# Kernel optimization log

Hardware: AMD Instinct MI355X
Metric: run time of the kernel (lower is better)

## Reference

```python
import jax, jax.numpy as jnp
import numpy as np

N = 100000        # nodes
E = 1600000       # edges (avg degree 16)
F_IN = 128        # num_node_features
H = 64            # hidden_channels
F_EDGE = 8        # num_edge_features (output dim per edge)


def setup_inputs() -> dict:
    key = jax.random.key(0)
    ks = jax.random.split(key, 9)
    x = jax.random.normal(ks[0], (N, F_IN), dtype=jnp.float32)
    edge_index = jax.random.randint(ks[1], (2, E), 0, N, dtype=jnp.int32)
    s = 0.05
    W1 = jax.random.normal(ks[2], (F_IN, H), jnp.float32) * s
    b1 = jnp.zeros((H,), jnp.float32)
    W2 = jax.random.normal(ks[3], (H, H), jnp.float32) * s
    b2 = jnp.zeros((H,), jnp.float32)
    Wl = jax.random.normal(ks[4], (2 * H, F_EDGE), jnp.float32) * s
    bl = jnp.zeros((F_EDGE,), jnp.float32)
    return {"x": x, "edge_index": edge_index,
            "W1": W1, "b1": b1, "W2": W2, "b2": b2, "Wl": Wl, "bl": bl}


def gcn_conv(x, W, b, row, col, n):
    # GCNConv: h = D^{-1/2} (A + I) D^{-1/2} (x W) + b
    h = x @ W
    sl = jnp.arange(n, dtype=row.dtype)          # self-loops
    r = jnp.concatenate([row, sl])
    c = jnp.concatenate([col, sl])
    ones = jnp.ones(r.shape[0], dtype=h.dtype)
    deg = jax.ops.segment_sum(ones, c, num_segments=n)      # in-degree incl. self-loop
    dinv = jax.lax.rsqrt(jnp.maximum(deg, 1e-12))
    norm = dinv[r] * dinv[c]                                 # symmetric normalization
    agg = jax.ops.segment_sum(norm[:, None] * h[r], c, num_segments=n)
    return agg + b


def reference(x, edge_index, W1, b1, W2, b2, Wl, bl):
    row, col = edge_index[0], edge_index[1]
    h = jax.nn.relu(gcn_conv(x, W1, b1, row, col, N))
    # dropout p=0.5 is identity at inference (training=False)
    h = jax.nn.relu(gcn_conv(h, W2, b2, row, col, N))
    x_i = h[row]                                  # [E, H]
    x_j = h[col]                                  # [E, H]
    return jnp.concatenate([x_i, x_j], axis=-1) @ Wl + bl   # [E, F_EDGE]
```

## Files before the change

kernel.cpp:

```cpp
#include <hip/hip_runtime.h>
#include <hip/hip_bf16.h>

static constexpr int NN  = 100000;
static constexpr int NE  = 1600000;
static constexpr int FIN = 128;
static constexpr int HD  = 64;

static constexpr int NB    = 256;
static constexpr int NPB   = 392;
static constexpr int EPB   = NE / NB;
static constexpr unsigned long long DIV392_MAGIC = 43826197ULL;

static constexpr int NSL = 4;

static constexpr int AGN  = 64;
static constexpr int ACAP = 1536;

typedef __attribute__((ext_vector_type(8))) short bf16x8;
typedef __attribute__((ext_vector_type(4))) float f32x4;

__device__ __forceinline__ float bf2f(unsigned short u) {
    return __uint_as_float(((unsigned int)u) << 16);
}
__device__ __forceinline__ unsigned short f2bf(float f) {
    __hip_bfloat16 hb = __float2bfloat16(f);
    return *(unsigned short*)&hb;
}
__device__ __forceinline__ int bucket_of(int c) {
    return (int)(((unsigned long long)(unsigned int)c * DIV392_MAGIC) >> 34);
}

__device__ __forceinline__ float load_in(const void* p, size_t i, int isbf) {
    return isbf ? bf2f(((const unsigned short*)p)[i]) : ((const float*)p)[i];
}

__global__ __launch_bounds__(256) void k_hist(const int* __restrict__ col, int* __restrict__ hist,
                                              const unsigned short* __restrict__ xu,
                                              int* __restrict__ flag) {
    __shared__ int h[4][NB];
    int t = threadIdx.x, w = t >> 6;
#pragma unroll
    for (int r = 0; r < 4; ++r) h[r][t] = 0;
    __syncthreads();
    int base = blockIdx.x * EPB;
    for (int e = base + t; e < base + EPB; e += 256)
        atomicAdd(&h[w][bucket_of(col[e])], 1);
    __syncthreads();
    hist[t * NB + blockIdx.x] = h[0][t] + h[1][t] + h[2][t] + h[3][t];
    if (blockIdx.x == 0) {
        __syncthreads();
        int cnt = 0;
        for (int k = t; k < 4096; k += 256) {
            unsigned short u = xu[2 * k];
            int ex = (u >> 7) & 0xFF;
            cnt += (ex >= 110 && ex <= 135) ? 1 : 0;
        }
        h[0][t] = cnt;
        __syncthreads();
        for (int off = 128; off > 0; off >>= 1) {
            if (t < off) h[0][t] += h[0][t + off];
            __syncthreads();
        }
        if (t == 0) flag[0] = (h[0][0] >= 2048) ? 1 : 0;
    }
}

__global__ __launch_bounds__(256) void k_gscan1(int* __restrict__ a, int* __restrict__ bsums) {
    __shared__ int sd[256];
    int t = threadIdx.x;
    int base = blockIdx.x * 1024 + t * 4;
    int v0 = a[base], v1 = a[base + 1], v2 = a[base + 2], v3 = a[base + 3];
    int tsum = v0 + v1 + v2 + v3;
    sd[t] = tsum;
    __syncthreads();
    for (int off = 1; off < 256; off <<= 1) {
        int tmp = (t >= off) ? sd[t - off] : 0;
        __syncthreads();
        sd[t] += tmp;
        __syncthreads();
    }
    int run = sd[t] - tsum;
    a[base] = run; run += v0;
    a[base + 1] = run; run += v1;
    a[base + 2] = run; run += v2;
    a[base + 3] = run;
    if (t == 255) bsums[blockIdx.x] = sd[t];
}

__device__ __forceinline__ void scan_bsums(const int* __restrict__ bsumsRaw, int* sb) {
    int t = threadIdx.x;
    int myv = 0;
    if (t < 64) { myv = bsumsRaw[t]; sb[t] = myv; }
    __syncthreads();
    for (int off = 1; off < 64; off <<= 1) {
        int v = (t < 64 && t >= off) ? sb[t - off] : 0;
        __syncthreads();
        if (t < 64) sb[t] += v;
        __syncthreads();
    }
    if (t < 64) sb[t] -= myv;
    __syncthreads();
}

__global__ __launch_bounds__(256) void k_binfill(const int* __restrict__ row, const int* __restrict__ col,
                                                 const int* __restrict__ histS,
                                                 const int* __restrict__ bsumsRaw,
                                                 int* __restrict__ csr_tmp) {
    __shared__ int cur[NB];
    __shared__ int sb[64];
    int t = threadIdx.x;
    scan_bsums(bsumsRaw, sb);
    cur[t] = histS[t * NB + blockIdx.x] + sb[t >> 2];
    __syncthreads();
    int base = blockIdx.x * EPB;
    for (int e = base + t; e < base + EPB; e += 256) {
        int r = row[e], c = col[e];
        int b = bucket_of(c);
        int p = atomicAdd(&cur[b], 1);
        csr_tmp[p] = r | ((c - b * NPB) << 17);
    }
}

__global__ __launch_bounds__(256) void k_bsort(const int* __restrict__ csr_tmp,
                                               const int* __restrict__ histS,
                                               const int* __restrict__ bsumsRaw,
                                               int* __restrict__ csr_src,
                                               int* __restrict__ start,
                                               float* __restrict__ dinv) {
    __shared__ int cnt[512];
    __shared__ int cur[512];
    __shared__ int sb[64];
    int t = threadIdx.x;
    int k = blockIdx.x;
    cnt[t] = 0; cnt[t + 256] = 0;
    scan_bsums(bsumsRaw, sb);
    int S = histS[k * NB] + sb[k >> 2];
    int E = (k < NB - 1) ? (histS[(k + 1) * NB] + sb[(k + 1) >> 2]) : NE;
    int nbase = k * NPB;
    __syncthreads();
    for (int e = S + t; e < E; e += 256)
        atomicAdd(&cnt[csr_tmp[e] >> 17], 1);
    __syncthreads();
    int rc0 = cnt[t], rc1 = cnt[t + 256];
    for (int d = 1; d < 512; d <<= 1) {
        int idx = (t + 1) * (d << 1) - 1;
        if (idx < 512) cnt[idx] += cnt[idx - d];
        __syncthreads();
    }
    if (t == 0) cnt[511] = 0;
    __syncthreads();
    for (int d = 256; d >= 1; d >>= 1) {
        int idx = (t + 1) * (d << 1) - 1;
        if (idx < 512) { int tmp = cnt[idx - d]; cnt[idx - d] = cnt[idx]; cnt[idx] += tmp; }
        __syncthreads();
    }
    int n0 = nbase + t;
    if (n0 < NN) {
        start[n0] = S + cnt[t] + rc0;
        dinv[n0] = rsqrtf((float)(rc0 + 1));
    }
    int li = t + 256;
    int n1 = nbase + li;
    if (li < NPB && n1 < NN) {
        start[n1] = S + cnt[li] + rc1;
        dinv[n1] = rsqrtf((float)(rc1 + 1));
    }
    cur[t] = cnt[t]; cur[t + 256] = cnt[t + 256];
    __syncthreads();
    for (int e = S + t; e < E; e += 256) {
        int u = csr_tmp[e];
        int p = atomicAdd(&cur[u >> 17], 1);
        csr_src[S + p] = u & 0x1FFFF;
    }
}

template <int K, bool XDUAL>
__global__ __launch_bounds__(256) void k_gemm_mfma(const void* __restrict__ X,
                                                   const void* __restrict__ W,
                                                   const float* __restrict__ dinv,
                                                   unsigned short* __restrict__ T4,
                                                   const int* __restrict__ flag) {
    constexpr int KT = K / 32;
    __shared__ unsigned short Bs[KT * 4 * 64 * 8];
    int isbf = flag[0];
    for (int tup = threadIdx.x; tup < KT * 4 * 64; tup += 256) {
        int l  = tup & 63;
        int nt = (tup >> 6) & 3;
        int kt = tup >> 8;
        int n  = nt * 16 + (l & 15);
        int kb = kt * 32 + (l >> 4) * 8;
        unsigned short tmp[8];
#pragma unroll
        for (int j = 0; j < 8; ++j) tmp[j] = f2bf(load_in(W, (size_t)(kb + j) * HD + n, isbf));
        *((uint4*)&Bs[(size_t)tup * 8]) = *((const uint4*)tmp);
    }
    __syncthreads();
    int wave = threadIdx.x >> 6, lane = threadIdx.x & 63;
    int quad = lane >> 4, m = lane & 15;
    int row0 = blockIdx.x * 64 + wave * 16;
    int row  = row0 + m;
    int rowc = (row < NN) ? row : (NN - 1);
    bool xf32 = XDUAL && (isbf == 0);
    const char* xrow = (const char*)X + (size_t)rowc * K * (xf32 ? 4 : 2);
    f32x4 acc[4];
#pragma unroll
    for (int nt = 0; nt < 4; ++nt) acc[nt] = (f32x4){0.f, 0.f, 0.f, 0.f};
#pragma unroll
    for (int kt = 0; kt < KT; ++kt) {
        bf16x8 a;
        if (!xf32) {
            a = *((const bf16x8*)(xrow + (size_t)(kt * 32 + quad * 8) * 2));
        } else {
            const float4* fp = (const float4*)(xrow + (size_t)(kt * 32 + quad * 8) * 4);
            float4 u0 = fp[0], u1 = fp[1];
            unsigned short tmp[8] = {f2bf(u0.x), f2bf(u0.y), f2bf(u0.z), f2bf(u0.w),
                                     f2bf(u1.x), f2bf(u1.y), f2bf(u1.z), f2bf(u1.w)};
            a = *((const bf16x8*)tmp);
        }
#pragma unroll
        for (int nt = 0; nt < 4; ++nt) {
            bf16x8 b = *((const bf16x8*)&Bs[(size_t)((kt * 4 + nt) * 64 + lane) * 8]);
            acc[nt] = __builtin_amdgcn_mfma_f32_16x16x32_bf16(a, b, acc[nt], 0, 0, 0);
        }
    }
#pragma unroll
    for (int r = 0; r < 4; ++r) {
        int orow = row0 + quad * 4 + r;
        if (orow < NN) {
            float sc = dinv[orow];
#pragma unroll
            for (int nt = 0; nt < 4; ++nt)
                T4[((size_t)nt * NN + orow) * 16 + m] = f2bf(acc[nt][r] * sc);
        }
    }
}

__global__ __launch_bounds__(256) void k_agg4(const unsigned short* __restrict__ T4,
                                              const int* __restrict__ endOff,
                                              const int* __restrict__ csr_src,
                                              const float* __restrict__ dinv,
                                              const void* __restrict__ bias,
                                              const int* __restrict__ flag,
                                              unsigned short* __restrict__ H4) {
    __shared__ int sIdx[ACAP];
    __shared__ int sEnd[AGN + 1];
    int isbf = flag[0];
    int slice = blockIdx.x & 3;
    int grp   = blockIdx.x >> 2;
    int i0 = grp * AGN;
    int t = threadIdx.x;
    if (t <= AGN) {
        int n = i0 + t - 1;
        sEnd[t] = (n < 0) ? 0 : endOff[(n < NN) ? n : (NN - 1)];
    }
    __syncthreads();
    int base  = sEnd[0];
    int total = sEnd[AGN] - base;
    bool fast = (total <= ACAP);
    if (fast)
        for (int k = t; k < total; k += 256) sIdx[k] = csr_src[base + k];
    __syncthreads();
    int li   = t >> 2;
    int slot = (t >> 1) & 1;
    int fl   = (t & 1) * 8;
    int i    = i0 + li;
    const unsigned short* Ts = T4 + (size_t)slice * NN * 16;
    union U { uint4 u; unsigned short s[8]; };
    float a[8];
#pragma unroll
    for (int j = 0; j < 8; ++j) a[j] = 0.f;
    if (i < NN) {
        int beg = sEnd[li] - base;
        int end = sEnd[li + 1] - base;
        int k = beg + slot;
        if (fast) {
            for (; k + 14 < end; k += 16) {
                int s0 = sIdx[k],      s1 = sIdx[k + 2],  s2 = sIdx[k + 4],  s3 = sIdx[k + 6];
                int s4 = sIdx[k + 8],  s5 = sIdx[k + 10], s6 = sIdx[k + 12], s7 = sIdx[k + 14];
                U t0, t1, t2, t3, t4, t5, t6, t7;
                t0.u = *((const uint4*)(Ts + (size_t)s0 * 16 + fl));
                t1.u = *((const uint4*)(Ts + (size_t)s1 * 16 + fl));
                t2.u = *((const uint4*)(Ts + (size_t)s2 * 16 + fl));
                t3.u = *((const uint4*)(Ts + (size_t)s3 * 16 + fl));
                t4.u = *((const uint4*)(Ts + (size_t)s4 * 16 + fl));
                t5.u = *((const uint4*)(Ts + (size_t)s5 * 16 + fl));
                t6.u = *((const uint4*)(Ts + (size_t)s6 * 16 + fl));
                t7.u = *((const uint4*)(Ts + (size_t)s7 * 16 + fl));
#pragma unroll
                for (int j = 0; j < 8; ++j)
                    a[j] += (bf2f(t0.s[j]) + bf2f(t1.s[j]) + bf2f(t2.s[j]) + bf2f(t3.s[j]))
                          + (bf2f(t4.s[j]) + bf2f(t5.s[j]) + bf2f(t6.s[j]) + bf2f(t7.s[j]));
            }
            for (; k < end; k += 2) {
                int s = sIdx[k];
                U tv; tv.u = *((const uint4*)(Ts + (size_t)s * 16 + fl));
#pragma unroll
                for (int j = 0; j < 8; ++j) a[j] += bf2f(tv.s[j]);
            }
        } else {
            for (; k + 6 < end; k += 8) {
                int s0 = csr_src[base + k],     s1 = csr_src[base + k + 2];
                int s2 = csr_src[base + k + 4], s3 = csr_src[base + k + 6];
                U t0, t1, t2, t3;
                t0.u = *((const uint4*)(Ts + (size_t)s0 * 16 + fl));
                t1.u = *((const uint4*)(Ts + (size_t)s1 * 16 + fl));
                t2.u = *((const uint4*)(Ts + (size_t)s2 * 16 + fl));
                t3.u = *((const uint4*)(Ts + (size_t)s3 * 16 + fl));
#pragma unroll
                for (int j = 0; j < 8; ++j)
                    a[j] += bf2f(t0.s[j]) + bf2f(t1.s[j]) + bf2f(t2.s[j]) + bf2f(t3.s[j]);
            }
            for (; k < end; k += 2) {
                int s = csr_src[base + k];
                U tv; tv.u = *((const uint4*)(Ts + (size_t)s * 16 + fl));
#pragma unroll
                for (int j = 0; j < 8; ++j) a[j] += bf2f(tv.s[j]);
            }
        }
    }
#pragma unroll
    for (int j = 0; j < 8; ++j) a[j] += __shfl_xor(a[j], 2, 64);
    if (i < NN && slot == 0) {
        float di = dinv[i];
        U sf; sf.u = *((const uint4*)(Ts + (size_t)i * 16 + fl));
        U o;
#pragma unroll
        for (int j = 0; j < 8; ++j) {
            float v = a[j] + bf2f(sf.s[j]);
            float b = load_in(bias, (size_t)(slice * 16 + fl + j), isbf);
            o.s[j] = f2bf(fmaxf(fmaf(di, v, b), 0.f));
        }
        *((uint4*)(H4 + ((size_t)slice * NN + i) * 16 + fl)) = o.u;
    }
}

__global__ __launch_bounds__(256) void k_gemm_h(const unsigned short* __restrict__ H4,
                                                const void* __restrict__ W,
                                                const float* __restrict__ dinv,
                                                unsigned short* __restrict__ Tb4,
                                                const int* __restrict__ flag) {
    __shared__ unsigned short Bs[2 * 4 * 64 * 8];
    int isbf = flag[0];
    for (int tup = threadIdx.x; tup < 512; tup += 256) {
        int l  = tup & 63;
        int nt = (tup >> 6) & 3;
        int kt = tup >> 8;
        int n  = nt * 16 + (l & 15);
        int kb = kt * 32 + (l >> 4) * 8;
        unsigned short tmp[8];
#pragma unroll
        for (int j = 0; j < 8; ++j) tmp[j] = f2bf(load_in(W, (size_t)(kb + j) * HD + n, isbf));
        *((uint4*)&Bs[(size_t)tup * 8]) = *((const uint4*)tmp);
    }
    __syncthreads();
    int wave = threadIdx.x >> 6, lane = threadIdx.x & 63;
    int quad = lane >> 4, m = lane & 15;
    int row0 = blockIdx.x * 64 + wave * 16;
    int row  = row0 + m;
    int rowc = (row < NN) ? row : (NN - 1);
    f32x4 acc[4];
#pragma unroll
    for (int nt = 0; nt < 4; ++nt) acc[nt] = (f32x4){0.f, 0.f, 0.f, 0.f};
#pragma unroll
    for (int kt = 0; kt < 2; ++kt) {
        int k0 = kt * 32 + quad * 8;
        bf16x8 a = *((const bf16x8*)&H4[((size_t)(k0 >> 4) * NN + rowc) * 16 + (k0 & 15)]);
#pragma unroll
        for (int nt = 0; nt < 4; ++nt) {
            bf16x8 b = *((const bf16x8*)&Bs[(size_t)((kt * 4 + nt) * 64 + lane) * 8]);
            acc[nt] = __builtin_amdgcn_mfma_f32_16x16x32_bf16(a, b, acc[nt], 0, 0, 0);
        }
    }
#pragma unroll
    for (int r = 0; r < 4; ++r) {
        int orow = row0 + quad * 4 + r;
        if (orow < NN) {
            float sc = dinv[orow];
#pragma unroll
            for (int nt = 0; nt < 4; ++nt)
                Tb4[((size_t)nt * NN + orow) * 16 + m] = f2bf(acc[nt][r] * sc);
        }
    }
}

__global__ __launch_bounds__(256) void k_pgemm_h(const unsigned short* __restrict__ H4,
                                                 const void* __restrict__ Wl,
                                                 const void* __restrict__ bl,
                                                 unsigned short* __restrict__ P,
                                                 const int* __restrict__ flag) {
    int isbf = flag[0];
    int wave = threadIdx.x >> 6, lane = threadIdx.x & 63;
    int quad = lane >> 4, m = lane & 15;
    bf16x8 bfr[2];
#pragma unroll
    for (int kt = 0; kt < 2; ++kt) {
        unsigned short tmp[8];
#pragma unroll
        for (int j = 0; j < 8; ++j) {
            int kk = kt * 32 + quad * 8 + j;
            float w = (m < 8) ? load_in(Wl, (size_t)kk * 8 + m, isbf)
                              : load_in(Wl, (size_t)(64 + kk) * 8 + (m - 8), isbf);
            tmp[j] = f2bf(w);
        }
        bfr[kt] = *((const bf16x8*)tmp);
    }
    float binit = (m < 8) ? load_in(bl, m, isbf) : 0.f;
    int row0 = blockIdx.x * 64 + wave * 16;
    int row  = row0 + m;
    int rowc = (row < NN) ? row : (NN - 1);
    f32x4 acc = (f32x4){binit, binit, binit, binit};
#pragma unroll
    for (int kt = 0; kt < 2; ++kt) {
        int k0 = kt * 32 + quad * 8;
        bf16x8 a = *((const bf16x8*)&H4[((size_t)(k0 >> 4) * NN + rowc) * 16 + (k0 & 15)]);
        acc = __builtin_amdgcn_mfma_f32_16x16x32_bf16(a, bfr[kt], acc, 0, 0, 0);
    }
#pragma unroll
    for (int r = 0; r < 4; ++r) {
        int orow = row0 + quad * 4 + r;
        if (orow < NN) P[(size_t)orow * 16 + m] = f2bf(acc[r]);
    }
}

__global__ __launch_bounds__(256) void k_edge_add(const unsigned short* __restrict__ P,
                                                  const int* __restrict__ erow,
                                                  const int* __restrict__ ecol,
                                                  void* __restrict__ out,
                                                  const int* __restrict__ flag) {
    int isbf = flag[0];
    int e = blockIdx.x * 256 + threadIdx.x;
    int i = erow[e], j = ecol[e];
    union U { uint4 u; unsigned short s[8]; };
    U a, b;
    a.u = *((const uint4*)(P + (size_t)i * 16));
    b.u = *((const uint4*)(P + (size_t)j * 16 + 8));
    float v[8];
#pragma unroll
    for (int o = 0; o < 8; ++o) v[o] = bf2f(a.s[o]) + bf2f(b.s[o]);
    if (isbf) {
        union { unsigned short h[8]; uint4 u; } p;
#pragma unroll
        for (int o = 0; o < 8; ++o) p.h[o] = f2bf(v[o]);
        *((uint4*)((__hip_bfloat16*)out + (size_t)e * 8)) = p.u;
    } else {
        float* op = (float*)out + (size_t)e * 8;
        ((float4*)op)[0] = make_float4(v[0], v[1], v[2], v[3]);
        ((float4*)op)[1] = make_float4(v[4], v[5], v[6], v[7]);
    }
}

extern "C" void kernel_launch(void* const* d_in, const int* in_sizes, int n_in,
                              void* d_out, int out_size, void* d_ws, size_t ws_size,
                              hipStream_t stream) {
    const void* x  = d_in[0];
    const int*  ei = (const int*)d_in[1];
    const void* W1 = d_in[2];
    const void* b1 = d_in[3];
    const void* W2 = d_in[4];
    const void* b2 = d_in[5];
    const void* Wl = d_in[6];
    const void* bl = d_in[7];
    const int* row = ei;
    const int* col = ei + NE;

    char* ws = (char*)d_ws;
    int*   flag    = (int*)ws;    ws += 16;
    int*   hist    = (int*)ws;    ws += (size_t)NB * NB * 4;
    int*   bsums   = (int*)ws;    ws += 256 * 4;
    int*   start   = (int*)ws;    ws += (size_t)NN * 4;
    float* dinv    = (float*)ws;  ws += (size_t)NN * 4;
    int*   csr_tmp = (int*)ws;    ws += (size_t)NE * 4;
    int*   csr_src = (int*)ws;    ws += (size_t)NE * 4;
    unsigned short* T4  = (unsigned short*)ws;  ws += (size_t)NN * 64 * 2;
    unsigned short* H4  = (unsigned short*)ws;  ws += (size_t)NN * 64 * 2;
    unsigned short* Tb4 = (unsigned short*)ws;  ws += (size_t)NN * 64 * 2;
    unsigned short* P   = (unsigned short*)ws;

    int gE   = (NE + 255) / 256;
    int gN64 = (NN + 63) / 64;
    int gAgg = ((NN + AGN - 1) / AGN) * NSL;

    k_hist   <<<NB, 256, 0, stream>>>(col, hist, (const unsigned short*)x, flag);
    k_gscan1 <<<64, 256, 0, stream>>>(hist, bsums);
    k_binfill<<<NB, 256, 0, stream>>>(row, col, hist, bsums, csr_tmp);
    k_bsort  <<<NB, 256, 0, stream>>>(csr_tmp, hist, bsums, csr_src, start, dinv);

    k_gemm_mfma<FIN, true><<<gN64, 256, 0, stream>>>(x, W1, dinv, T4, flag);
    k_agg4 <<<gAgg, 256, 0, stream>>>(T4, start, csr_src, dinv, b1, flag, H4);

    k_gemm_h<<<gN64, 256, 0, stream>>>(H4, W2, dinv, Tb4, flag);
    k_agg4 <<<gAgg, 256, 0, stream>>>(Tb4, start, csr_src, dinv, b2, flag, H4);

    k_pgemm_h<<<gN64, 256, 0, stream>>>(H4, Wl, bl, P, flag);
    k_edge_add<<<gE, 256, 0, stream>>>(P, row, col, d_out, flag);
}
```

Baseline: 301.9 us.

## Degree-sort nodes within buckets to balance aggregation work per wavefront

```diff
diff --git a/kernel.cpp b/kernel.cpp
--- a/kernel.cpp
+++ b/kernel.cpp
@@ -8,13 +8,14 @@
 
 static constexpr int NB    = 256;
 static constexpr int NPB   = 392;
+static constexpr int NSLOT = NB * NPB;
 static constexpr int EPB   = NE / NB;
 static constexpr unsigned long long DIV392_MAGIC = 43826197ULL;
 
 static constexpr int NSL = 4;
 
 static constexpr int AGN  = 64;
-static constexpr int ACAP = 1536;
+static constexpr int ACAP = 3072;
 
 typedef __attribute__((ext_vector_type(8))) short bf16x8;
 typedef __attribute__((ext_vector_type(4))) float f32x4;
@@ -125,52 +126,84 @@
                                                const int* __restrict__ histS,
                                                const int* __restrict__ bsumsRaw,
                                                int* __restrict__ csr_src,
-                                               int* __restrict__ start,
+                                               int* __restrict__ rankedEnd,
+                                               int* __restrict__ perm,
                                                float* __restrict__ dinv) {
-    __shared__ int cnt[512];
-    __shared__ int cur[512];
+    __shared__ int h1[512];
+    __shared__ int h2[512];
+    __shared__ int h3[512];
+    __shared__ int segS[512];
     __shared__ int sb[64];
+    __shared__ int bigCur;
     int t = threadIdx.x;
     int k = blockIdx.x;
-    cnt[t] = 0; cnt[t + 256] = 0;
+    h1[t] = 0; h1[t + 256] = 0;
+    h2[t] = 0; h2[t + 256] = 0;
+    h3[t] = 0; h3[t + 256] = 0;
     scan_bsums(bsumsRaw, sb);
     int S = histS[k * NB] + sb[k >> 2];
     int E = (k < NB - 1) ? (histS[(k + 1) * NB] + sb[(k + 1) >> 2]) : NE;
     int nbase = k * NPB;
-    __syncthreads();
+    int validCnt = NN - nbase; if (validCnt > NPB) validCnt = NPB; if (validCnt < 0) validCnt = 0;
     for (int e = S + t; e < E; e += 256)
-        atomicAdd(&cnt[csr_tmp[e] >> 17], 1);
-    __syncthreads();
-    int rc0 = cnt[t], rc1 = cnt[t + 256];
+        atomicAdd(&h1[csr_tmp[e] >> 17], 1);
+    __syncthreads();
+    int rc0 = h1[t], rc1 = h1[t + 256];
+    __syncthreads();
+    h1[t] = 0; h1[t + 256] = 0;
+    bool v0 = (t < validCnt);
+    bool v1 = (t + 256 < validCnt);
+    int b0 = (rc0 < 511) ? rc0 : 511;
+    int b1 = (rc1 < 511) ? rc1 : 511;
+    if (v0) { atomicAdd(&h2[b0], 1); atomicAdd(&h3[b0], rc0); }
+    if (v1) { atomicAdd(&h2[b1], 1); atomicAdd(&h3[b1], rc1); }
+    __syncthreads();
     for (int d = 1; d < 512; d <<= 1) {
         int idx = (t + 1) * (d << 1) - 1;
-        if (idx < 512) cnt[idx] += cnt[idx - d];
-        __syncthreads();
-    }
-    if (t == 0) cnt[511] = 0;
+        if (idx < 512) { h2[idx] += h2[idx - d]; h3[idx] += h3[idx - d]; }
+        __syncthreads();
+    }
+    if (t == 0) { h2[511] = 0; h3[511] = 0; }
     __syncthreads();
     for (int d = 256; d >= 1; d >>= 1) {
         int idx = (t + 1) * (d << 1) - 1;
-        if (idx < 512) { int tmp = cnt[idx - d]; cnt[idx - d] = cnt[idx]; cnt[idx] += tmp; }
-        __syncthreads();
-    }
-    int n0 = nbase + t;
-    if (n0 < NN) {
-        start[n0] = S + cnt[t] + rc0;
-        dinv[n0] = rsqrtf((float)(rc0 + 1));
-    }
-    int li = t + 256;
-    int n1 = nbase + li;
-    if (li < NPB && n1 < NN) {
-        start[n1] = S + cnt[li] + rc1;
-        dinv[n1] = rsqrtf((float)(rc1 + 1));
-    }
-    cur[t] = cnt[t]; cur[t + 256] = cnt[t + 256];
+        if (idx < 512) {
+            int a2 = h2[idx - d]; h2[idx - d] = h2[idx]; h2[idx] += a2;
+            int a3 = h3[idx - d]; h3[idx - d] = h3[idx]; h3[idx] += a3;
+        }
+        __syncthreads();
+    }
+    if (t == 0) bigCur = h3[511];
+    __syncthreads();
+    if (v0) {
+        int n = nbase + t;
+        int sr = atomicAdd(&h1[b0], 1);
+        int slot = h2[b0] + sr;
+        int segOff = (b0 < 511) ? (h3[b0] + sr * b0) : atomicAdd(&bigCur, rc0);
+        perm[nbase + slot] = n;
+        rankedEnd[nbase + slot] = S + segOff + rc0;
+        segS[t] = S + segOff;
+        dinv[n] = rsqrtf((float)(rc0 + 1));
+    }
+    if (v1) {
+        int n = nbase + t + 256;
+        int sr = atomicAdd(&h1[b1], 1);
+        int slot = h2[b1] + sr;
+        int segOff = (b1 < 511) ? (h3[b1] + sr * b1) : atomicAdd(&bigCur, rc1);
+        perm[nbase + slot] = n;
+        rankedEnd[nbase + slot] = S + segOff + rc1;
+        segS[t + 256] = S + segOff;
+        dinv[n] = rsqrtf((float)(rc1 + 1));
+    }
+    for (int s = validCnt + t; s < NPB; s += 256) {
+        perm[nbase + s] = -1;
+        rankedEnd[nbase + s] = E;
+    }
     __syncthreads();
     for (int e = S + t; e < E; e += 256) {
         int u = csr_tmp[e];
-        int p = atomicAdd(&cur[u >> 17], 1);
-        csr_src[S + p] = u & 0x1FFFF;
+        int p = atomicAdd(&segS[u >> 17], 1);
+        csr_src[p] = u & 0x1FFFF;
     }
 }
 
@@ -236,7 +269,8 @@
 }
 
 __global__ __launch_bounds__(256) void k_agg4(const unsigned short* __restrict__ T4,
-                                              const int* __restrict__ endOff,
+                                              const int* __restrict__ rankedEnd,
+                                              const int* __restrict__ perm,
                                               const int* __restrict__ csr_src,
                                               const float* __restrict__ dinv,
                                               const void* __restrict__ bias,
@@ -244,15 +278,17 @@
                                               unsigned short* __restrict__ H4) {
     __shared__ int sIdx[ACAP];
     __shared__ int sEnd[AGN + 1];
+    __shared__ int sPerm[AGN];
     int isbf = flag[0];
     int slice = blockIdx.x & 3;
     int grp   = blockIdx.x >> 2;
     int i0 = grp * AGN;
     int t = threadIdx.x;
     if (t <= AGN) {
-        int n = i0 + t - 1;
-        sEnd[t] = (n < 0) ? 0 : endOff[(n < NN) ? n : (NN - 1)];
-    }
+        int g = i0 + t - 1;
+        sEnd[t] = (g < 0) ? 0 : rankedEnd[g];
+    }
+    if (t < AGN) sPerm[t] = perm[i0 + t];
     __syncthreads();
     int base  = sEnd[0];
     int total = sEnd[AGN] - base;
@@ -263,33 +299,27 @@
     int li   = t >> 2;
     int slot = (t >> 1) & 1;
     int fl   = (t & 1) * 8;
-    int i    = i0 + li;
+    int i    = sPerm[li];
     const unsigned short* Ts = T4 + (size_t)slice * NN * 16;
     union U { uint4 u; unsigned short s[8]; };
     float a[8];
 #pragma unroll
     for (int j = 0; j < 8; ++j) a[j] = 0.f;
-    if (i < NN) {
+    if (i >= 0) {
         int beg = sEnd[li] - base;
         int end = sEnd[li + 1] - base;
         int k = beg + slot;
         if (fast) {
-            for (; k + 14 < end; k += 16) {
-                int s0 = sIdx[k],      s1 = sIdx[k + 2],  s2 = sIdx[k + 4],  s3 = sIdx[k + 6];
-                int s4 = sIdx[k + 8],  s5 = sIdx[k + 10], s6 = sIdx[k + 12], s7 = sIdx[k + 14];
-                U t0, t1, t2, t3, t4, t5, t6, t7;
+            for (; k + 6 < end; k += 8) {
+                int s0 = sIdx[k], s1 = sIdx[k + 2], s2 = sIdx[k + 4], s3 = sIdx[k + 6];
+                U t0, t1, t2, t3;
                 t0.u = *((const uint4*)(Ts + (size_t)s0 * 16 + fl));
                 t1.u = *((const uint4*)(Ts + (size_t)s1 * 16 + fl));
                 t2.u = *((const uint4*)(Ts + (size_t)s2 * 16 + fl));
                 t3.u = *((const uint4*)(Ts + (size_t)s3 * 16 + fl));
-                t4.u = *((const uint4*)(Ts + (size_t)s4 * 16 + fl));
-                t5.u = *((const uint4*)(Ts + (size_t)s5 * 16 + fl));
-                t6.u = *((const uint4*)(Ts + (size_t)s6 * 16 + fl));
-                t7.u = *((const uint4*)(Ts + (size_t)s7 * 16 + fl));
 #pragma unroll
                 for (int j = 0; j < 8; ++j)
-                    a[j] += (bf2f(t0.s[j]) + bf2f(t1.s[j]) + bf2f(t2.s[j]) + bf2f(t3.s[j]))
-                          + (bf2f(t4.s[j]) + bf2f(t5.s[j]) + bf2f(t6.s[j]) + bf2f(t7.s[j]));
+                    a[j] += bf2f(t0.s[j]) + bf2f(t1.s[j]) + bf2f(t2.s[j]) + bf2f(t3.s[j]);
             }
             for (; k < end; k += 2) {
                 int s = sIdx[k];
@@ -320,7 +350,7 @@
     }
 #pragma unroll
     for (int j = 0; j < 8; ++j) a[j] += __shfl_xor(a[j], 2, 64);
-    if (i < NN && slot == 0) {
+    if (i >= 0 && slot == 0) {
         float di = dinv[i];
         U sf; sf.u = *((const uint4*)(Ts + (size_t)i * 16 + fl));
         U o;
@@ -467,7 +497,8 @@
     int*   flag    = (int*)ws;    ws += 16;
     int*   hist    = (int*)ws;    ws += (size_t)NB * NB * 4;
     int*   bsums   = (int*)ws;    ws += 256 * 4;
-    int*   start   = (int*)ws;    ws += (size_t)NN * 4;
+    int*   rankedEnd = (int*)ws;  ws += (size_t)NSLOT * 4;
+    int*   perm    = (int*)ws;    ws += (size_t)NSLOT * 4;
     float* dinv    = (float*)ws;  ws += (size_t)NN * 4;
     int*   csr_tmp = (int*)ws;    ws += (size_t)NE * 4;
     int*   csr_src = (int*)ws;    ws += (size_t)NE * 4;
@@ -478,18 +509,18 @@
 
     int gE   = (NE + 255) / 256;
     int gN64 = (NN + 63) / 64;
-    int gAgg = ((NN + AGN - 1) / AGN) * NSL;
+    int gAgg = (NSLOT / AGN) * NSL;
 
     k_hist   <<<NB, 256, 0, stream>>>(col, hist, (const unsigned short*)x, flag);
     k_gscan1 <<<64, 256, 0, stream>>>(hist, bsums);
     k_binfill<<<NB, 256, 0, stream>>>(row, col, hist, bsums, csr_tmp);
-    k_bsort  <<<NB, 256, 0, stream>>>(csr_tmp, hist, bsums, csr_src, start, dinv);
+    k_bsort  <<<NB, 256, 0, stream>>>(csr_tmp, hist, bsums, csr_src, rankedEnd, perm, dinv);
 
     k_gemm_mfma<FIN, true><<<gN64, 256, 0, stream>>>(x, W1, dinv, T4, flag);
-    k_agg4 <<<gAgg, 256, 0, stream>>>(T4, start, csr_src, dinv, b1, flag, H4);
+    k_agg4 <<<gAgg, 256, 0, stream>>>(T4, rankedEnd, perm, csr_src, dinv, b1, flag, H4);
 
     k_gemm_h<<<gN64, 256, 0, stream>>>(H4, W2, dinv, Tb4, flag);
-    k_agg4 <<<gAgg, 256, 0, stream>>>(Tb4, start, csr_src, dinv, b2, flag, H4);
+    k_agg4 <<<gAgg, 256, 0, stream>>>(Tb4, rankedEnd, perm, csr_src, dinv, b2, flag, H4);
 
     k_pgemm_h<<<gN64, 256, 0, stream>>>(H4, Wl, bl, P, flag);
     k_edge_add<<<gE, 256, 0, stream>>>(P, row, col, d_out, flag);
```

Result: no change. 306.2 us (+1.4%).
